# Optimization experiments

Hardware: AMD Instinct MI355X
Metric: run time of the kernel (lower is better)

The kernel has to match this reference:

```python
import jax, jax.numpy as jnp
import numpy as np

N_EMBD = 1024
N_HEAD = 16
HEAD_SIZE = N_EMBD // N_HEAD
B, T = 2, 2048
LN_EPS = 1e-5


def _layernorm(x, g, b):
    mu = jnp.mean(x, axis=-1, keepdims=True)
    var = jnp.var(x, axis=-1, keepdims=True)
    return (x - mu) * jax.lax.rsqrt(var + LN_EPS) * g + b


def setup_inputs() -> dict:
    key = jax.random.key(0)
    ks = jax.random.split(key, 12)
    s_in = 1.0 / np.sqrt(N_EMBD)
    s_ff = 1.0 / np.sqrt(4 * N_EMBD)
    return {
        "x": jax.random.normal(ks[0], (B, T, N_EMBD), jnp.float32),
        # per-head q/k/v linears stacked head-major: [n_embd, n_embd]
        "Wq": jax.random.uniform(ks[1], (N_EMBD, N_EMBD), jnp.float32, -s_in, s_in),
        "Wk": jax.random.uniform(ks[2], (N_EMBD, N_EMBD), jnp.float32, -s_in, s_in),
        "Wv": jax.random.uniform(ks[3], (N_EMBD, N_EMBD), jnp.float32, -s_in, s_in),
        "Wo": jax.random.uniform(ks[4], (N_EMBD, N_EMBD), jnp.float32, -s_in, s_in),
        "bo": jax.random.uniform(ks[5], (N_EMBD,), jnp.float32, -s_in, s_in),
        "W1": jax.random.uniform(ks[6], (N_EMBD, 4 * N_EMBD), jnp.float32, -s_in, s_in),
        "b1": jax.random.uniform(ks[7], (4 * N_EMBD,), jnp.float32, -s_in, s_in),
        "W2": jax.random.uniform(ks[8], (4 * N_EMBD, N_EMBD), jnp.float32, -s_ff, s_ff),
        "b2": jax.random.uniform(ks[9], (N_EMBD,), jnp.float32, -s_ff, s_ff),
        "g1": jnp.ones((N_EMBD,), jnp.float32),
        "be1": jnp.zeros((N_EMBD,), jnp.float32),
        "g2": jnp.ones((N_EMBD,), jnp.float32),
        "be2": jnp.zeros((N_EMBD,), jnp.float32),
    }


def reference(x, Wq, Wk, Wv, Wo, bo, W1, b1, W2, b2, g1, be1, g2, be2):
    Bx, Tx, C = x.shape
    # --- self-attention on ln1(x) ---
    h = _layernorm(x, g1, be1)
    q = (h @ Wq).reshape(Bx, Tx, N_HEAD, HEAD_SIZE)
    k = (h @ Wk).reshape(Bx, Tx, N_HEAD, HEAD_SIZE)
    v = (h @ Wv).reshape(Bx, Tx, N_HEAD, HEAD_SIZE)
    # NOTE: faithful to source -- scale uses full C (n_embd), not head_size
    scale = C ** (-0.5)
    wei = jnp.einsum("bqhd,bkhd->bhqk", q, k) * scale  # [B,H,T,T]
    causal = jnp.tril(jnp.ones((Tx, Tx), bool))
    wei = jnp.where(causal, wei, -jnp.inf)
    wei = jax.nn.softmax(wei, axis=-1)
    attn = jnp.einsum("bhqk,bkhd->bqhd", wei, v).reshape(Bx, Tx, C)
    x = x + (attn @ Wo + bo)
    # --- feed-forward on ln2(x) ---
    h2 = _layernorm(x, g2, be2)
    x = x + (jax.nn.relu(h2 @ W1 + b1) @ W2 + b2)
    return x
```

## Files before the change

kernel.cpp:

```cpp
#include <hip/hip_runtime.h>
#include <hip/hip_bf16.h>
#include <math.h>

#define BB 2
#define TT 2048
#define CC 1024
#define NH 16
#define HD 64
#define BT (BB*TT)
#define LN_EPS 1e-5f
#define ATT_SCALE 0.03125f

typedef __bf16 bf16x8 __attribute__((ext_vector_type(8)));
typedef __bf16 bf16x4 __attribute__((ext_vector_type(4)));
typedef short shortx4 __attribute__((ext_vector_type(4)));
typedef float floatx4 __attribute__((ext_vector_type(4)));

__device__ __forceinline__ void gl_lds16(const __bf16* g, __bf16* l) {
    __builtin_amdgcn_global_load_lds((const __attribute__((address_space(1))) void*)g,
                                     (__attribute__((address_space(3))) void*)l,
                                     16, 0, 0);
}

#define MFMA32(a, b, c) __builtin_amdgcn_mfma_f32_16x16x32_bf16(a, b, c, 0, 0, 0)

#if __has_builtin(__builtin_amdgcn_mfma_f32_16x16x16_bf16)
__device__ __forceinline__ floatx4 mfma16(bf16x4 a, bf16x4 b, floatx4 c) {
    return __builtin_amdgcn_mfma_f32_16x16x16_bf16(a, b, c, 0, 0, 0);
}
#else
__device__ __forceinline__ floatx4 mfma16(bf16x4 a, bf16x4 b, floatx4 c) {
    return __builtin_amdgcn_mfma_f32_16x16x16bf16_1k(
        __builtin_bit_cast(shortx4, a), __builtin_bit_cast(shortx4, b), c, 0, 0, 0);
}
#endif

#define BARRIER() __builtin_amdgcn_s_barrier()
#define MEMF()  asm volatile("" ::: "memory")
#define LGKM0() asm volatile("s_waitcnt lgkmcnt(0)" ::: "memory")
#define VM4()   asm volatile("s_waitcnt vmcnt(4)" ::: "memory")
#define VM0()   asm volatile("s_waitcnt vmcnt(0)" ::: "memory")

__device__ __forceinline__ void swizzle_xcd(int& xb, int& yb, int& zb) {
    int nx = gridDim.x, ny = gridDim.y;
    int total = nx * ny * (int)gridDim.z;
    int lin = blockIdx.x + nx * (blockIdx.y + ny * blockIdx.z);
    int c = lin & 7, s = lin >> 3;
    int idx = c * (total >> 3) + s;
    xb = idx % nx;
    yb = (idx / nx) % ny;
    zb = idx / (nx * ny);
}

__global__ __launch_bounds__(256) void transpose_ln(
        const float* __restrict__ Wq, const float* __restrict__ Wk,
        const float* __restrict__ Wv, const float* __restrict__ Wo,
        const float* __restrict__ W1, const float* __restrict__ W2,
        __bf16* __restrict__ WqkvT, __bf16* __restrict__ WoT,
        __bf16* __restrict__ W1T, __bf16* __restrict__ W2T,
        const float* __restrict__ x, const float* __restrict__ g1,
        const float* __restrict__ be1, __bf16* __restrict__ hb) {
    __shared__ float t[32][33];
    __shared__ float rs_[4], rss_[4];
    __shared__ float mu_s, inv_s;
    int idx = blockIdx.x;
    if (idx >= 12288) {
        int row = idx - 12288;
        const float4* xr = (const float4*)(x + (size_t)row * CC);
        float4 v = xr[threadIdx.x];
        float s  = v.x + v.y + v.z + v.w;
        float ss = v.x*v.x + v.y*v.y + v.z*v.z + v.w*v.w;
        #pragma unroll
        for (int off = 32; off; off >>= 1) {
            s  += __shfl_down(s, off);
            ss += __shfl_down(ss, off);
        }
        int lane = threadIdx.x & 63, wid = threadIdx.x >> 6;
        if (lane == 0) { rs_[wid] = s; rss_[wid] = ss; }
        __syncthreads();
        if (threadIdx.x == 0) {
            float S  = rs_[0] + rs_[1] + rs_[2] + rs_[3];
            float SS = rss_[0] + rss_[1] + rss_[2] + rss_[3];
            float mu  = S * (1.0f / CC);
            float var = SS * (1.0f / CC) - mu * mu;
            mu_s  = mu;
            inv_s = rsqrtf(var + LN_EPS);
        }
        __syncthreads();
        float mu = mu_s, inv = inv_s;
        float4 gv = ((const float4*)g1)[threadIdx.x];
        float4 bv = ((const float4*)be1)[threadIdx.x];
        bf16x4 o;
        o[0] = (__bf16)((v.x - mu) * inv * gv.x + bv.x);
        o[1] = (__bf16)((v.y - mu) * inv * gv.y + bv.y);
        o[2] = (__bf16)((v.z - mu) * inv * gv.z + bv.z);
        o[3] = (__bf16)((v.w - mu) * inv * gv.w + bv.w);
        *(bf16x4*)(hb + (size_t)row * CC + threadIdx.x * 4) = o;
        return;
    }
    const float* src; __bf16* dst; int K, N, tn, tk;
    if (idx < 3072) {
        int wsel = idx >> 10, local = idx & 1023;
        src = (wsel == 0) ? Wq : (wsel == 1 ? Wk : Wv);
        dst = WqkvT + (size_t)wsel * 1024 * 1024;
        K = 1024; N = 1024; tn = local & 31; tk = local >> 5;
    } else if (idx < 4096) {
        int local = idx - 3072;
        src = Wo; dst = WoT; K = 1024; N = 1024; tn = local & 31; tk = local >> 5;
    } else if (idx < 8192) {
        int local = idx - 4096;
        src = W1; dst = W1T; K = 1024; N = 4096; tn = local & 127; tk = local >> 7;
    } else {
        int local = idx - 8192;
        src = W2; dst = W2T; K = 4096; N = 1024; tn = local & 31; tk = local >> 5;
    }
    int n0 = tn * 32, k0 = tk * 32;
    int tx = threadIdx.x & 31, ty = threadIdx.x >> 5;
    #pragma unroll
    for (int r = ty; r < 32; r += 8)
        t[r][tx] = src[(size_t)(k0 + r) * N + n0 + tx];
    __syncthreads();
    #pragma unroll
    for (int r = ty; r < 32; r += 8)
        dst[(size_t)(n0 + r) * K + k0 + tx] = (__bf16)t[tx][r];
}

__global__ __launch_bounds__(256) void reduce_wo_ln(const __bf16* __restrict__ P,
                                                    const float* __restrict__ bo,
                                                    const float* __restrict__ x,
                                                    const float* __restrict__ g2,
                                                    const float* __restrict__ be2,
                                                    float* __restrict__ x2,
                                                    __bf16* __restrict__ hb) {
    int row = blockIdx.x;
    int c = threadIdx.x * 4;
    bf16x4 a0 = *(const bf16x4*)(P + (size_t)row * CC + c);
    bf16x4 a1 = *(const bf16x4*)(P + (size_t)BT * CC + (size_t)row * CC + c);
    float4 xb = *(const float4*)(x + (size_t)row * CC + c);
    float4 bb = *(const float4*)(bo + c);
    float4 v;
    v.x = xb.x + bb.x + (float)a0[0] + (float)a1[0];
    v.y = xb.y + bb.y + (float)a0[1] + (float)a1[1];
    v.z = xb.z + bb.z + (float)a0[2] + (float)a1[2];
    v.w = xb.w + bb.w + (float)a0[3] + (float)a1[3];
    *(float4*)(x2 + (size_t)row * CC + c) = v;

    float s  = v.x + v.y + v.z + v.w;
    float ss = v.x*v.x + v.y*v.y + v.z*v.z + v.w*v.w;
    #pragma unroll
    for (int off = 32; off; off >>= 1) {
        s  += __shfl_down(s, off);
        ss += __shfl_down(ss, off);
    }
    __shared__ float rs_[4], rss_[4];
    __shared__ float mu_s, inv_s;
    int lane = threadIdx.x & 63, wid = threadIdx.x >> 6;
    if (lane == 0) { rs_[wid] = s; rss_[wid] = ss; }
    __syncthreads();
    if (threadIdx.x == 0) {
        float S  = rs_[0] + rs_[1] + rs_[2] + rs_[3];
        float SS = rss_[0] + rss_[1] + rss_[2] + rss_[3];
        float mu  = S * (1.0f / CC);
        float var = SS * (1.0f / CC) - mu * mu;
        mu_s  = mu;
        inv_s = rsqrtf(var + LN_EPS);
    }
    __syncthreads();
    float mu = mu_s, inv = inv_s;
    float4 gv = ((const float4*)g2)[threadIdx.x];
    float4 bv = ((const float4*)be2)[threadIdx.x];
    bf16x4 o;
    o[0] = (__bf16)((v.x - mu) * inv * gv.x + bv.x);
    o[1] = (__bf16)((v.y - mu) * inv * gv.y + bv.y);
    o[2] = (__bf16)((v.z - mu) * inv * gv.z + bv.z);
    o[3] = (__bf16)((v.w - mu) * inv * gv.w + bv.w);
    *(bf16x4*)(hb + (size_t)row * CC + c) = o;
}

__global__ __launch_bounds__(256) void reduce_ffn(const __bf16* __restrict__ P,
                                                  const float* __restrict__ b2,
                                                  const float* __restrict__ x2,
                                                  float* __restrict__ out) {
    int row = blockIdx.x;
    int c = threadIdx.x * 4;
    const size_t S = (size_t)BT * CC;
    float4 v = *(const float4*)(x2 + (size_t)row * CC + c);
    float4 bb = *(const float4*)(b2 + c);
    v.x += bb.x; v.y += bb.y; v.z += bb.z; v.w += bb.w;
    #pragma unroll
    for (int z = 0; z < 4; ++z) {
        bf16x4 a = *(const bf16x4*)(P + z * S + (size_t)row * CC + c);
        v.x += (float)a[0]; v.y += (float)a[1]; v.z += (float)a[2]; v.w += (float)a[3];
    }
    *(float4*)(out + (size_t)row * CC + c) = v;
}

struct Frags { bf16x8 a[4][2]; bf16x8 b[2][2]; };

__device__ __forceinline__ void stage_half(const __bf16* __restrict__ mat, int row0,
                                           int ldk, int k0, __bf16* lds, int tid) {
    int r = tid >> 3;
    int lch = (tid & 7) ^ (r & 7);
    const __bf16* gp = mat + (size_t)(row0 + r) * ldk + k0 + lch * 8;
    gl_lds16(gp, lds + tid * 8);
    gl_lds16(gp + (size_t)64 * ldk, lds + 4096 + tid * 8);
}

template<int QR, int QC>
__device__ __forceinline__ void phase_loads(const __bf16* As_, const __bf16* Bs_,
                                            int wr, int wc, int m, int g, Frags& f) {
    #pragma unroll
    for (int i = 0; i < 4; ++i) {
        int ra = QR * 128 + wr * 64 + i * 16 + m;
        #pragma unroll
        for (int kk = 0; kk < 2; ++kk)
            f.a[i][kk] = *(const bf16x8*)&As_[ra * 64 + (((kk * 4 + g) ^ (m & 7)) * 8)];
    }
    #pragma unroll
    for (int j = 0; j < 2; ++j) {
        int rb = QC * 128 + wc * 32 + j * 16 + m;
        #pragma unroll
        for (int kk = 0; kk < 2; ++kk)
            f.b[j][kk] = *(const bf16x8*)&Bs_[rb * 64 + (((kk * 4 + g) ^ (m & 7)) * 8)];
    }
}

template<int QR, int QC>
__device__ __forceinline__ void phase_mfma(Frags& f, floatx4 (&acc)[2][2][4][2]) {
    __builtin_amdgcn_s_setprio(1);
    #pragma unroll
    for (int i = 0; i < 4; ++i)
        #pragma unroll
        for (int j = 0; j < 2; ++j)
            #pragma unroll
            for (int kk = 0; kk < 2; ++kk)
                acc[QR][QC][i][j] = MFMA32(f.a[i][kk], f.b[j][kk], acc[QR][QC][i][j]);
    __builtin_amdgcn_s_setprio(0);
}

template<int SK, typename OT, bool BIAS, bool RELU, bool VSPLIT>
__global__ __launch_bounds__(512, 2) void gemm256(const __bf16* __restrict__ A,
                                                  const __bf16* __restrict__ Bt,
                                                  const float* __restrict__ bias,
                                                  OT* __restrict__ C,
                                                  __bf16* __restrict__ vt,
                                                  int M, int N, int K) {
    __shared__ __bf16 As[2][16384];
    __shared__ __bf16 Bs[2][16384];
    int bx, by, bz;
    swizzle_xcd(bx, by, bz);
    const int tid = threadIdx.x;
    const int l = tid & 63, w = tid >> 6;
    const int m = l & 15, g = l >> 4;
    const int wr = w >> 2, wc = w & 3;
    const int m0 = by * 256, n0 = bx * 256;
    const int Keff = K / SK;
    const int kb = (SK > 1) ? bz * Keff : 0;
    const int iters = Keff >> 7;

    floatx4 acc[2][2][4][2];
    #pragma unroll
    for (int a = 0; a < 2; ++a)
        #pragma unroll
        for (int b = 0; b < 2; ++b)
            #pragma unroll
            for (int i = 0; i < 4; ++i)
                #pragma unroll
                for (int j = 0; j < 2; ++j) {
                    floatx4 z = {0.f, 0.f, 0.f, 0.f};
                    acc[a][b][i][j] = z;
                }

    stage_half(A,  m0,       K, kb,      &As[0][0],    tid);
    stage_half(Bt, n0,       K, kb,      &Bs[0][0],    tid);
    stage_half(Bt, n0 + 128, K, kb,      &Bs[0][8192], tid);
    stage_half(A,  m0 + 128, K, kb,      &As[0][8192], tid);
    stage_half(A,  m0,       K, kb + 64, &As[1][0],    tid);
    stage_half(Bt, n0 + 128, K, kb + 64, &Bs[1][8192], tid);
    VM4(); BARRIER(); MEMF();

    for (int it = 0; it < iters; ++it) {
        const bool lastI = (it == iters - 1);
        const int kB = kb + (2 * it + 1) * 64;
        const int kC = kB + 64;
        const int kD = kC + 64;

        { Frags f; phase_loads<0,0>(&As[0][0], &Bs[0][0], wr, wc, m, g, f);
          stage_half(Bt, n0, K, kB, &Bs[1][0], tid);
          BARRIER(); LGKM0(); phase_mfma<0,0>(f, acc); BARRIER(); MEMF(); }
        { Frags f; phase_loads<0,1>(&As[0][0], &Bs[0][0], wr, wc, m, g, f);
          stage_half(A, m0 + 128, K, kB, &As[1][8192], tid);
          BARRIER(); LGKM0(); phase_mfma<0,1>(f, acc); BARRIER(); MEMF(); }
        { Frags f; phase_loads<1,1>(&As[0][0], &Bs[0][0], wr, wc, m, g, f);
          if (!lastI) stage_half(A, m0, K, kC, &As[0][0], tid);
          BARRIER(); LGKM0(); phase_mfma<1,1>(f, acc); BARRIER(); MEMF(); }
        { Frags f; phase_loads<1,0>(&As[0][0], &Bs[0][0], wr, wc, m, g, f);
          if (!lastI) { stage_half(Bt, n0 + 128, K, kC, &Bs[0][8192], tid);
                        VM4(); }
          else VM0();
          BARRIER(); LGKM0(); phase_mfma<1,0>(f, acc); BARRIER(); MEMF(); }
        { Frags f; phase_loads<0,0>(&As[1][0], &Bs[1][0], wr, wc, m, g, f);
          if (!lastI) stage_half(Bt, n0, K, kC, &Bs[0][0], tid);
          BARRIER(); LGKM0(); phase_mfma<0,0>(f, acc); BARRIER(); MEMF(); }
        { Frags f; phase_loads<0,1>(&As[1][0], &Bs[1][0], wr, wc, m, g, f);
          if (!lastI) stage_half(A, m0 + 128, K, kC, &As[0][8192], tid);
          BARRIER(); LGKM0(); phase_mfma<0,1>(f, acc); BARRIER(); MEMF(); }
        { Frags f; phase_loads<1,1>(&As[1][0], &Bs[1][0], wr, wc, m, g, f);
          if (!lastI) stage_half(A, m0, K, kD, &As[1][0], tid);
          BARRIER(); LGKM0(); phase_mfma<1,1>(f, acc); BARRIER(); MEMF(); }
        { Frags f; phase_loads<1,0>(&As[1][0], &Bs[1][0], wr, wc, m, g, f);
          if (!lastI) { stage_half(Bt, n0 + 128, K, kD, &Bs[1][8192], tid);
                        VM4(); }
          BARRIER(); LGKM0(); phase_mfma<1,0>(f, acc); BARRIER(); MEMF(); }
    }

    if (SK > 1) {
        __bf16* P = (__bf16*)C + (size_t)bz * M * N;
        #pragma unroll
        for (int qr = 0; qr < 2; ++qr)
            #pragma unroll
            for (int i = 0; i < 4; ++i) {
                int row = m0 + qr * 128 + wr * 64 + i * 16 + g * 4;
                #pragma unroll
                for (int qc = 0; qc < 2; ++qc)
                    #pragma unroll
                    for (int j = 0; j < 2; ++j) {
                        int col = n0 + qc * 128 + wc * 32 + j * 16 + m;
                        #pragma unroll
                        for (int r = 0; r < 4; ++r)
                            P[(size_t)(row + r) * N + col] = (__bf16)acc[qr][qc][i][j][r];
                    }
            }
    } else if (VSPLIT && n0 >= 2048) {
        #pragma unroll
        for (int qr = 0; qr < 2; ++qr)
            #pragma unroll
            for (int i = 0; i < 4; ++i) {
                int row = m0 + qr * 128 + wr * 64 + i * 16 + g * 4;
                int bb = row >> 11, t0 = row & 2047;
                #pragma unroll
                for (int qc = 0; qc < 2; ++qc)
                    #pragma unroll
                    for (int j = 0; j < 2; ++j) {
                        int cv = n0 + qc * 128 + wc * 32 + j * 16 + m - 2048;
                        bf16x4 o;
                        #pragma unroll
                        for (int r = 0; r < 4; ++r) o[r] = (__bf16)acc[qr][qc][i][j][r];
                        *(bf16x4*)(vt + ((size_t)(bb * NH + (cv >> 6)) * HD + (cv & 63)) * 2048 + t0) = o;
                    }
            }
    } else {
        #pragma unroll
        for (int qr = 0; qr < 2; ++qr)
            #pragma unroll
            for (int i = 0; i < 4; ++i) {
                int row = m0 + qr * 128 + wr * 64 + i * 16 + g * 4;
                #pragma unroll
                for (int qc = 0; qc < 2; ++qc)
                    #pragma unroll
                    for (int j = 0; j < 2; ++j) {
                        int col = n0 + qc * 128 + wc * 32 + j * 16 + m;
                        float bv = BIAS ? bias[col] : 0.0f;
                        #pragma unroll
                        for (int r = 0; r < 4; ++r) {
                            float vo = acc[qr][qc][i][j][r] + bv;
                            if (RELU) vo = fmaxf(vo, 0.0f);
                            C[(size_t)(row + r) * N + col] = (OT)vo;
                        }
                    }
            }
    }
}

__global__ __launch_bounds__(256, 2) void attn_mfma3(const __bf16* __restrict__ qkv,
                                                     const __bf16* __restrict__ vt,
                                                     __bf16* __restrict__ att) {
    const int lin = blockIdx.x;
    const int half = lin >> 8, pid = lin & 255;
    const int q0 = pid & 7, h = (pid >> 3) & 15, b = pid >> 7;
    const int qt = half ? 15 - q0 : q0;

    const int tid = threadIdx.x;
    const int l = tid & 63, w = tid >> 6;
    const int m = l & 15, g = l >> 4;

    __shared__ __bf16 Ks[2][128][32];
    __shared__ __bf16 Vt3[8][64][16];

    const __bf16* qp = qkv + (size_t)b * TT * 3072 + h * HD;
    const __bf16* kp = qp + 1024;
    const __bf16* vh = vt + (size_t)(b * NH + h) * HD * 2048;

    bf16x8 qb[2][2];
    #pragma unroll
    for (int nt = 0; nt < 2; ++nt) {
        int qrow = qt * 128 + w * 32 + nt * 16 + m;
        qb[nt][0] = *(const bf16x8*)(qp + (size_t)qrow * 3072 + g * 8);
        qb[nt][1] = *(const bf16x8*)(qp + (size_t)qrow * 3072 + 32 + g * 8);
    }

    floatx4 O[2][4];
    float l_s[2] = {0.0f, 0.0f};
    #pragma unroll
    for (int nt = 0; nt < 2; ++nt)
        #pragma unroll
        for (int jd = 0; jd < 4; ++jd) {
            floatx4 z = {0.f, 0.f, 0.f, 0.f};
            O[nt][jd] = z;
        }

    for (int kt = 0; kt <= qt; ++kt) {
        __syncthreads();
        #pragma unroll
        for (int c = 0; c < 4; ++c) {
            int idx = w * 4 + c;
            int dh = idx >> 3, k16 = idx & 7;
            gl_lds16(kp + (size_t)(kt * 128 + k16 * 16 + (l >> 2)) * 3072
                        + dh * 32 + (((l & 3) ^ ((l >> 3) & 3)) * 8),
                     (__bf16*)Ks + dh * 4096 + k16 * 512);
        }
        #pragma unroll
        for (int c = 0; c < 4; ++c) {
            int idx = w * 4 + c;
            int jt = idx >> 1, dhf = idx & 1;
            gl_lds16(vh + (size_t)(dhf * 32 + (l >> 1)) * 2048 + kt * 128
                        + jt * 16 + (((l & 1) ^ ((l >> 3) & 1)) * 8),
                     (__bf16*)Vt3 + jt * 1024 + dhf * 512);
        }
        __syncthreads();

        floatx4 S[2][8];
        #pragma unroll
        for (int jt = 0; jt < 8; ++jt) {
            int co = (g ^ ((m >> 1) & 3)) * 8;
            bf16x8 kf0 = *(const bf16x8*)&Ks[0][jt * 16 + m][co];
            bf16x8 kf1 = *(const bf16x8*)&Ks[1][jt * 16 + m][co];
            #pragma unroll
            for (int nt = 0; nt < 2; ++nt) {
                floatx4 z = {0.f, 0.f, 0.f, 0.f};
                z = MFMA32(kf0, qb[nt][0], z);
                S[nt][jt] = MFMA32(kf1, qb[nt][1], z);
            }
        }

        bf16x4 pv[2][8];
        const bool last = (kt == qt);
        #pragma unroll
        for (int nt = 0; nt < 2; ++nt) {
            if (last) {
                int qr = w * 32 + nt * 16 + m;
                #pragma unroll
                for (int jt = 0; jt < 8; ++jt)
                    #pragma unroll
                    for (int r = 0; r < 4; ++r)
                        if (jt * 16 + g * 4 + r > qr) S[nt][jt][r] = -1e30f;
            }
            float ls = 0.0f;
            #pragma unroll
            for (int jt = 0; jt < 8; ++jt) {
                bf16x4 t;
                #pragma unroll
                for (int r = 0; r < 4; ++r) {
                    float p = __expf(S[nt][jt][r] * ATT_SCALE);
                    ls += p;
                    t[r] = (__bf16)p;
                }
                pv[nt][jt] = t;
            }
            l_s[nt] += ls;
        }

        #pragma unroll
        for (int jt = 0; jt < 8; ++jt)
            #pragma unroll
            for (int jd = 0; jd < 4; ++jd) {
                bf16x4 vf = *(const bf16x4*)&Vt3[jt][jd * 16 + m]
                                [((g >> 1) ^ ((m >> 2) & 1)) * 8 + (g & 1) * 4];
                #pragma unroll
                for (int nt = 0; nt < 2; ++nt)
                    O[nt][jd] = mfma16(vf, pv[nt][jt], O[nt][jd]);
            }
    }

    #pragma unroll
    for (int nt = 0; nt < 2; ++nt) {
        float lsum = l_s[nt];
        lsum += __shfl_xor(lsum, 16, 64);
        lsum += __shfl_xor(lsum, 32, 64);
        float inv = 1.0f / lsum;
        int qrow = qt * 128 + w * 32 + nt * 16 + m;
        #pragma unroll
        for (int jd = 0; jd < 4; ++jd) {
            bf16x4 o;
            #pragma unroll
            for (int r = 0; r < 4; ++r) o[r] = (__bf16)(O[nt][jd][r] * inv);
            *(bf16x4*)(att + ((size_t)b * TT + qrow) * CC + h * HD + jd * 16 + g * 4) = o;
        }
    }
}

extern "C" void kernel_launch(void* const* d_in, const int* in_sizes, int n_in,
                              void* d_out, int out_size, void* d_ws, size_t ws_size,
                              hipStream_t stream) {
    const float* x   = (const float*)d_in[0];
    const float* Wq  = (const float*)d_in[1];
    const float* Wk  = (const float*)d_in[2];
    const float* Wv  = (const float*)d_in[3];
    const float* Wo  = (const float*)d_in[4];
    const float* bo  = (const float*)d_in[5];
    const float* W1  = (const float*)d_in[6];
    const float* b1  = (const float*)d_in[7];
    const float* W2  = (const float*)d_in[8];
    const float* b2  = (const float*)d_in[9];
    const float* g1  = (const float*)d_in[10];
    const float* be1 = (const float*)d_in[11];
    const float* g2  = (const float*)d_in[12];
    const float* be2 = (const float*)d_in[13];
    float* out = (float*)d_out;

    char* p = (char*)d_ws;
    char*   pool  = p;          p += (size_t)32 * 1024 * 1024;
    __bf16* qkvb  = (__bf16*)pool;
    __bf16* vtb   = (__bf16*)(pool + (size_t)BT * 3072 * 2);
    __bf16* wop   = (__bf16*)pool;
    __bf16* ffp   = (__bf16*)pool;
    __bf16* attb  = (__bf16*)p; p += (size_t)BT * CC * 2;
    __bf16* hb    = (__bf16*)p; p += (size_t)BT * CC * 2;
    float*  x2    = (float*)p;  p += (size_t)BT * CC * 4;
    __bf16* ffb   = (__bf16*)p; p += (size_t)BT * 4096 * 2;
    __bf16* WqkvT = (__bf16*)p; p += (size_t)3072 * 1024 * 2;
    __bf16* WoT   = (__bf16*)p; p += (size_t)1024 * 1024 * 2;
    __bf16* W1T   = (__bf16*)p; p += (size_t)4096 * 1024 * 2;
    __bf16* W2T   = (__bf16*)p; p += (size_t)1024 * 4096 * 2;

    transpose_ln<<<16384, 256, 0, stream>>>(Wq, Wk, Wv, Wo, W1, W2,
                                            WqkvT, WoT, W1T, W2T,
                                            x, g1, be1, hb);
    gemm256<1, __bf16, false, false, true><<<dim3(12, 16), 512, 0, stream>>>(
        hb, WqkvT, nullptr, qkvb, vtb, BT, 3072, 1024);
    attn_mfma3<<<512, 256, 0, stream>>>(qkvb, vtb, attb);
    gemm256<2, __bf16, false, false, false><<<dim3(4, 16, 2), 512, 0, stream>>>(
        attb, WoT, nullptr, wop, nullptr, BT, 1024, 1024);
    reduce_wo_ln<<<BT, 256, 0, stream>>>(wop, bo, x, g2, be2, x2, hb);
    gemm256<1, __bf16, true, true, false><<<dim3(16, 16), 512, 0, stream>>>(
        hb, W1T, b1, ffb, nullptr, BT, 4096, 1024);
    gemm256<4, __bf16, false, false, false><<<dim3(4, 16, 4), 512, 0, stream>>>(
        ffb, W2T, nullptr, ffp, nullptr, BT, 1024, 4096);
    reduce_ffn<<<BT, 256, 0, stream>>>(ffp, b2, x2, out);
}
```

Before: 356.0 us.

## Reuse A/B register fragments across GEMM quadrants and split-K the Wo GEMM by four

The GEMM main loop now keeps A and B fragments in registers and reuses them across quadrants: A for row-half 0 is shared by two column quadrants, and the B fragments are kept for the later row-half. This removes redundant LDS reads and lets one phase skip its fragment loads entirely. Separately, the Wo projection goes from split-K 2 to split-K 4, which raises the block count. reduce_wo_ln is updated to sum four partials, at the cost of extra partial-buffer traffic and more live registers.

```diff
diff --git a/kernel.cpp b/kernel.cpp
--- a/kernel.cpp
+++ b/kernel.cpp
@@ -134,15 +134,19 @@
                                                     __bf16* __restrict__ hb) {
     int row = blockIdx.x;
     int c = threadIdx.x * 4;
-    bf16x4 a0 = *(const bf16x4*)(P + (size_t)row * CC + c);
-    bf16x4 a1 = *(const bf16x4*)(P + (size_t)BT * CC + (size_t)row * CC + c);
+    const size_t S = (size_t)BT * CC;
     float4 xb = *(const float4*)(x + (size_t)row * CC + c);
     float4 bb = *(const float4*)(bo + c);
     float4 v;
-    v.x = xb.x + bb.x + (float)a0[0] + (float)a1[0];
-    v.y = xb.y + bb.y + (float)a0[1] + (float)a1[1];
-    v.z = xb.z + bb.z + (float)a0[2] + (float)a1[2];
-    v.w = xb.w + bb.w + (float)a0[3] + (float)a1[3];
+    v.x = xb.x + bb.x;
+    v.y = xb.y + bb.y;
+    v.z = xb.z + bb.z;
+    v.w = xb.w + bb.w;
+    #pragma unroll
+    for (int z = 0; z < 4; ++z) {
+        bf16x4 a = *(const bf16x4*)(P + z * S + (size_t)row * CC + c);
+        v.x += (float)a[0]; v.y += (float)a[1]; v.z += (float)a[2]; v.w += (float)a[3];
+    }
     *(float4*)(x2 + (size_t)row * CC + c) = v;
 
     float s  = v.x + v.y + v.z + v.w;
@@ -158,9 +162,9 @@
     if (lane == 0) { rs_[wid] = s; rss_[wid] = ss; }
     __syncthreads();
     if (threadIdx.x == 0) {
-        float S  = rs_[0] + rs_[1] + rs_[2] + rs_[3];
+        float S_  = rs_[0] + rs_[1] + rs_[2] + rs_[3];
         float SS = rss_[0] + rss_[1] + rss_[2] + rss_[3];
-        float mu  = S * (1.0f / CC);
+        float mu  = S_ * (1.0f / CC);
         float var = SS * (1.0f / CC) - mu * mu;
         mu_s  = mu;
         inv_s = rsqrtf(var + LN_EPS);
@@ -195,8 +199,6 @@
     *(float4*)(out + (size_t)row * CC + c) = v;
 }
 
-struct Frags { bf16x8 a[4][2]; bf16x8 b[2][2]; };
-
 __device__ __forceinline__ void stage_half(const __bf16* __restrict__ mat, int row0,
                                            int ldk, int k0, __bf16* lds, int tid) {
     int r = tid >> 3;
@@ -206,27 +208,30 @@
     gl_lds16(gp + (size_t)64 * ldk, lds + 4096 + tid * 8);
 }
 
-template<int QR, int QC>
-__device__ __forceinline__ void phase_loads(const __bf16* As_, const __bf16* Bs_,
-                                            int wr, int wc, int m, int g, Frags& f) {
+__device__ __forceinline__ void load_a(const __bf16* As_, int qr, int wr, int m, int g,
+                                       bf16x8 (&fa)[4][2]) {
     #pragma unroll
     for (int i = 0; i < 4; ++i) {
-        int ra = QR * 128 + wr * 64 + i * 16 + m;
+        int ra = qr * 128 + wr * 64 + i * 16 + m;
         #pragma unroll
         for (int kk = 0; kk < 2; ++kk)
-            f.a[i][kk] = *(const bf16x8*)&As_[ra * 64 + (((kk * 4 + g) ^ (m & 7)) * 8)];
-    }
+            fa[i][kk] = *(const bf16x8*)&As_[ra * 64 + (((kk * 4 + g) ^ (m & 7)) * 8)];
+    }
+}
+
+__device__ __forceinline__ void load_b(const __bf16* Bs_, int qc, int wc, int m, int g,
+                                       bf16x8 (&fb)[2][2]) {
     #pragma unroll
     for (int j = 0; j < 2; ++j) {
-        int rb = QC * 128 + wc * 32 + j * 16 + m;
+        int rb = qc * 128 + wc * 32 + j * 16 + m;
         #pragma unroll
         for (int kk = 0; kk < 2; ++kk)
-            f.b[j][kk] = *(const bf16x8*)&Bs_[rb * 64 + (((kk * 4 + g) ^ (m & 7)) * 8)];
-    }
-}
-
-template<int QR, int QC>
-__device__ __forceinline__ void phase_mfma(Frags& f, floatx4 (&acc)[2][2][4][2]) {
+            fb[j][kk] = *(const bf16x8*)&Bs_[rb * 64 + (((kk * 4 + g) ^ (m & 7)) * 8)];
+    }
+}
+
+__device__ __forceinline__ void mfma_q(bf16x8 (&fa)[4][2], bf16x8 (&fb)[2][2],
+                                       floatx4 (&a)[4][2]) {
     __builtin_amdgcn_s_setprio(1);
     #pragma unroll
     for (int i = 0; i < 4; ++i)
@@ -234,7 +239,7 @@
         for (int j = 0; j < 2; ++j)
             #pragma unroll
             for (int kk = 0; kk < 2; ++kk)
-                acc[QR][QC][i][j] = MFMA32(f.a[i][kk], f.b[j][kk], acc[QR][QC][i][j]);
+                a[i][j] = MFMA32(fa[i][kk], fb[j][kk], a[i][j]);
     __builtin_amdgcn_s_setprio(0);
 }
 
@@ -279,39 +284,42 @@
     stage_half(Bt, n0 + 128, K, kb + 64, &Bs[1][8192], tid);
     VM4(); BARRIER(); MEMF();
 
+    bf16x8 fa[4][2], fbA[2][2], fbB[2][2];
+
     for (int it = 0; it < iters; ++it) {
         const bool lastI = (it == iters - 1);
         const int kB = kb + (2 * it + 1) * 64;
         const int kC = kB + 64;
         const int kD = kC + 64;
 
-        { Frags f; phase_loads<0,0>(&As[0][0], &Bs[0][0], wr, wc, m, g, f);
-          stage_half(Bt, n0, K, kB, &Bs[1][0], tid);
-          BARRIER(); LGKM0(); phase_mfma<0,0>(f, acc); BARRIER(); MEMF(); }
-        { Frags f; phase_loads<0,1>(&As[0][0], &Bs[0][0], wr, wc, m, g, f);
-          stage_half(A, m0 + 128, K, kB, &As[1][8192], tid);
-          BARRIER(); LGKM0(); phase_mfma<0,1>(f, acc); BARRIER(); MEMF(); }
-        { Frags f; phase_loads<1,1>(&As[0][0], &Bs[0][0], wr, wc, m, g, f);
-          if (!lastI) stage_half(A, m0, K, kC, &As[0][0], tid);
-          BARRIER(); LGKM0(); phase_mfma<1,1>(f, acc); BARRIER(); MEMF(); }
-        { Frags f; phase_loads<1,0>(&As[0][0], &Bs[0][0], wr, wc, m, g, f);
-          if (!lastI) { stage_half(Bt, n0 + 128, K, kC, &Bs[0][8192], tid);
-                        VM4(); }
-          else VM0();
-          BARRIER(); LGKM0(); phase_mfma<1,0>(f, acc); BARRIER(); MEMF(); }
-        { Frags f; phase_loads<0,0>(&As[1][0], &Bs[1][0], wr, wc, m, g, f);
-          if (!lastI) stage_half(Bt, n0, K, kC, &Bs[0][0], tid);
-          BARRIER(); LGKM0(); phase_mfma<0,0>(f, acc); BARRIER(); MEMF(); }
-        { Frags f; phase_loads<0,1>(&As[1][0], &Bs[1][0], wr, wc, m, g, f);
-          if (!lastI) stage_half(A, m0 + 128, K, kC, &As[0][8192], tid);
-          BARRIER(); LGKM0(); phase_mfma<0,1>(f, acc); BARRIER(); MEMF(); }
-        { Frags f; phase_loads<1,1>(&As[1][0], &Bs[1][0], wr, wc, m, g, f);
-          if (!lastI) stage_half(A, m0, K, kD, &As[1][0], tid);
-          BARRIER(); LGKM0(); phase_mfma<1,1>(f, acc); BARRIER(); MEMF(); }
-        { Frags f; phase_loads<1,0>(&As[1][0], &Bs[1][0], wr, wc, m, g, f);
-          if (!lastI) { stage_half(Bt, n0 + 128, K, kD, &Bs[1][8192], tid);
-                        VM4(); }
-          BARRIER(); LGKM0(); phase_mfma<1,0>(f, acc); BARRIER(); MEMF(); }
+        load_a(&As[0][0], 0, wr, m, g, fa);
+        load_b(&Bs[0][0], 0, wc, m, g, fbA);
+        stage_half(Bt, n0, K, kB, &Bs[1][0], tid);
+        BARRIER(); LGKM0(); mfma_q(fa, fbA, acc[0][0]); BARRIER(); MEMF();
+        load_b(&Bs[0][0], 1, wc, m, g, fbB);
+        stage_half(A, m0 + 128, K, kB, &As[1][8192], tid);
+        BARRIER(); LGKM0(); mfma_q(fa, fbB, acc[0][1]); BARRIER(); MEMF();
+        load_a(&As[0][0], 1, wr, m, g, fa);
+        if (!lastI) stage_half(A, m0, K, kC, &As[0][0], tid);
+        BARRIER(); LGKM0(); mfma_q(fa, fbB, acc[1][1]); BARRIER(); MEMF();
+        if (!lastI) { stage_half(Bt, n0 + 128, K, kC, &Bs[0][8192], tid);
+                      VM4(); }
+        else VM0();
+        BARRIER(); mfma_q(fa, fbA, acc[1][0]); BARRIER(); MEMF();
+
+        load_a(&As[1][0], 0, wr, m, g, fa);
+        load_b(&Bs[1][0], 0, wc, m, g, fbA);
+        if (!lastI) stage_half(Bt, n0, K, kC, &Bs[0][0], tid);
+        BARRIER(); LGKM0(); mfma_q(fa, fbA, acc[0][0]); BARRIER(); MEMF();
+        load_b(&Bs[1][0], 1, wc, m, g, fbB);
+        if (!lastI) stage_half(A, m0 + 128, K, kC, &As[0][8192], tid);
+        BARRIER(); LGKM0(); mfma_q(fa, fbB, acc[0][1]); BARRIER(); MEMF();
+        load_a(&As[1][0], 1, wr, m, g, fa);
+        if (!lastI) stage_half(A, m0, K, kD, &As[1][0], tid);
+        BARRIER(); LGKM0(); mfma_q(fa, fbB, acc[1][1]); BARRIER(); MEMF();
+        if (!lastI) { stage_half(Bt, n0 + 128, K, kD, &Bs[1][8192], tid);
+                      VM4(); }
+        BARRIER(); mfma_q(fa, fbA, acc[1][0]); BARRIER(); MEMF();
     }
 
     if (SK > 1) {
@@ -539,7 +547,7 @@
     gemm256<1, __bf16, false, false, true><<<dim3(12, 16), 512, 0, stream>>>(
         hb, WqkvT, nullptr, qkvb, vtb, BT, 3072, 1024);
     attn_mfma3<<<512, 256, 0, stream>>>(qkvb, vtb, attb);
-    gemm256<2, __bf16, false, false, false><<<dim3(4, 16, 2), 512, 0, stream>>>(
+    gemm256<4, __bf16, false, false, false><<<dim3(4, 16, 4), 512, 0, stream>>>(
         attb, WoT, nullptr, wop, nullptr, BT, 1024, 1024);
     reduce_wo_ln<<<BT, 256, 0, stream>>>(wop, bo, x, g2, be2, x2, hb);
     gemm256<1, __bf16, true, true, false><<<dim3(16, 16), 512, 0, stream>>>(
```

Result: faster. 329.2 us (-7.5%).
